# Performance work log

Hardware: AMD Instinct MI355X
Metric: run time of the kernel (lower is better)

Reference implementation:

```python
import jax, jax.numpy as jnp
import numpy as np
import math

_DENSE_LOCAL_W = 64
_DYADIC = [96, 128, 192, 256, 384, 512, 768, 1024, 1536]
OFFSETS = sorted(set(range(0, _DENSE_LOCAL_W + 1)) | set(_DYADIC))  # 74 offsets

B, N, D, H = 1, 2048, 1024, 16
HD = D // H


def setup_inputs() -> dict:
    key = jax.random.key(0)
    ks = jax.random.split(key, 8)
    s = 1.0 / math.sqrt(D)
    x = jax.random.normal(ks[0], (B, N, D), dtype=jnp.float32)
    Wqkv = jax.random.uniform(ks[1], (3 * D, D), jnp.float32, -s, s)
    bqkv = jax.random.uniform(ks[2], (3 * D,), jnp.float32, -s, s)
    Wgate = jax.random.uniform(ks[3], (D, D), jnp.float32, -s, s)
    bgate = jax.random.uniform(ks[4], (D,), jnp.float32, -s, s)
    Wout = jax.random.uniform(ks[5], (D, D), jnp.float32, -s, s)
    bout = jax.random.uniform(ks[6], (D,), jnp.float32, -s, s)
    # pos_bias init exactly as in the module: -log(1+delta) * alpha_h, shape (O, H)
    alphas = jnp.linspace(0.2, 2.0, H)
    deltas = jnp.array([math.log(1.0 + d) for d in OFFSETS], dtype=jnp.float32)
    pos_bias = -deltas[:, None] * alphas[None, :]
    offsets = jnp.array(OFFSETS, dtype=jnp.int32)
    return {"x": x, "Wqkv": Wqkv, "bqkv": bqkv, "Wgate": Wgate, "bgate": bgate,
            "Wout": Wout, "bout": bout, "pos_bias": pos_bias, "offsets": offsets}


def reference(x, Wqkv, bqkv, Wgate, bgate, Wout, bout, pos_bias, offsets):
    Bx, Nx, Dx = x.shape
    qkv = x @ Wqkv.T + bqkv                       # (B, N, 3D)
    q, k, v = jnp.split(qkv, 3, axis=-1)
    q = q.reshape(Bx, Nx, H, HD).transpose(0, 2, 1, 3)  # (B, H, N, HD)
    k = k.reshape(Bx, Nx, H, HD).transpose(0, 2, 1, 3)
    v = v.reshape(Bx, Nx, H, HD).transpose(0, 2, 1, 3)
    scale = HD ** -0.5

    # gather shifted K/V: position n attends to n - delta for each fixed offset
    n_idx = jnp.arange(Nx, dtype=jnp.int32)[:, None]      # (N, 1)
    idx = n_idx - offsets[None, :]                        # (N, O)
    valid = idx >= 0                                      # (N, O)
    idx_c = jnp.clip(idx, 0, Nx - 1)
    K_all = k[:, :, idx_c, :]                             # (B, H, N, O, HD)
    V_all = v[:, :, idx_c, :]

    scores = jnp.einsum('bhnd,bhnod->bhno', q, K_all) * scale
    scores = scores + pos_bias.T[None, :, None, :]        # (1, H, 1, O)
    scores = jnp.where(valid[None, None], scores, -jnp.inf)
    alpha = jax.nn.softmax(scores, axis=-1)               # (B, H, N, O)
    out = jnp.einsum('bhno,bhnod->bhnd', alpha, V_all)    # (B, H, N, HD)

    flat = out.transpose(0, 2, 1, 3).reshape(Bx, Nx, Dx)  # (B, N, D)
    gate = jax.nn.sigmoid(x @ Wgate.T + bgate)
    return (flat * gate) @ Wout.T + bout                  # dropout = identity (eval)
```

## Files before the change

### kernel.cpp

```cpp
#include <hip/hip_runtime.h>
#include <hip/hip_bf16.h>

#define SEQ_N 2048
#define DIM   1024
#define NHEAD 16
#define HDIM  64
#define LDQ   4096
#define NOFF  74
#define NDENSE 65
#define NJ    224
#define NT    16
#define PST   232
#define QST   88

typedef __attribute__((ext_vector_type(8))) __bf16 bv8;
typedef __attribute__((ext_vector_type(4))) __bf16 bv4;
typedef __attribute__((ext_vector_type(4))) float  f32x4;

typedef __attribute__((address_space(3))) void as3_void;
typedef __attribute__((address_space(1))) void as1_void;

__device__ __forceinline__ void async16(const void* g, void* l) {
  __builtin_amdgcn_global_load_lds((as1_void*)(unsigned long long)g,
                                   (as3_void*)l, 16, 0, 0);
}

#define E1 (SEQ_N * DIM)
#define E2 (E1 + 3 * DIM * DIM)
#define E3 (E2 + DIM * DIM)
#define E4 (E3 + DIM * DIM)
__global__ __launch_bounds__(256) void cvt_all(
    const float* __restrict__ x, const float* __restrict__ wqkv,
    const float* __restrict__ wgate, const float* __restrict__ wout,
    __bf16* __restrict__ dst) {
  long i = ((long)blockIdx.x * 256 + threadIdx.x) * 4;
  if (i >= E4) return;
  const float* s; long o;
  if (i < E1)      { s = x;     o = i; }
  else if (i < E2) { s = wqkv;  o = i - E1; }
  else if (i < E3) { s = wgate; o = i - E2; }
  else             { s = wout;  o = i - E3; }
  float4 v = *(const float4*)(s + o);
  bv4 ov;
  ov[0] = (__bf16)v.x; ov[1] = (__bf16)v.y; ov[2] = (__bf16)v.z; ov[3] = (__bf16)v.w;
  *(bv4*)(dst + i) = ov;
}

#define BM 128
#define BKT 128

template <int BN_, typename OutT>
__global__ __launch_bounds__(256) void gemm_bt(
    const __bf16* __restrict__ A, const __bf16* __restrict__ B1,
    const __bf16* __restrict__ B2, const float* __restrict__ bias1,
    const float* __restrict__ bias2, int Nsplit,
    OutT* __restrict__ C, int ldc, int K) {
  __shared__ __attribute__((aligned(16))) __bf16 Asm[BM * BKT];
  __shared__ __attribute__((aligned(16))) __bf16 Bsm[BN_ * BKT];
  constexpr int NJT = BN_ / 32;
  constexpr int CA = BM * BKT / 8;
  constexpr int CB = BN_ * BKT / 8;
  constexpr int CPR = BKT / 8;

  const int tid  = threadIdx.x;
  const int lane = tid & 63;
  const int wave = tid >> 6;
  const int wr = wave >> 1, wc = wave & 1;
  const int fr = lane & 15, fq = lane >> 4;
  const int fr7 = fr & 7;

  const int bn0 = blockIdx.x * BN_;
  const int bm0 = blockIdx.y * BM;

  const __bf16* Bp;
  const float* biasp;
  if (bn0 < Nsplit) { Bp = B1 + (size_t)bn0 * K;            biasp = bias1 + bn0; }
  else              { Bp = B2 + (size_t)(bn0 - Nsplit) * K; biasp = bias2 + (bn0 - Nsplit); }
  const __bf16* Ap = A + (size_t)bm0 * K;

  f32x4 acc[4][NJT] = {};

  for (int kt = 0; kt < K; kt += BKT) {
    __syncthreads();
#pragma unroll
    for (int c0 = 0; c0 < CA + CB; c0 += 256) {
      int c = c0 + tid;
      if (c < CA) {
        int rr = c / CPR, qq = c % CPR;
        int qs = qq ^ (rr & 7);
        async16(Ap + (size_t)rr * K + kt + qs * 8, Asm + c * 8);
      } else {
        int cb = c - CA;
        int rr = cb / CPR, qq = cb % CPR;
        int qs = qq ^ (rr & 7);
        async16(Bp + (size_t)rr * K + kt + qs * 8, Bsm + cb * 8);
      }
    }
    __syncthreads();

#pragma unroll
    for (int kk = 0; kk < BKT / 32; ++kk) {
      const int qs = ((kk * 4 + fq) ^ fr7) * 8;
      bv8 af[4], bfr[NJT];
#pragma unroll
      for (int i = 0; i < 4; ++i)
        af[i] = *(const bv8*)(Asm + (wr * 64 + i * 16 + fr) * BKT + qs);
#pragma unroll
      for (int j = 0; j < NJT; ++j)
        bfr[j] = *(const bv8*)(Bsm + (wc * (BN_ / 2) + j * 16 + fr) * BKT + qs);
#pragma unroll
      for (int i = 0; i < 4; ++i)
#pragma unroll
        for (int j = 0; j < NJT; ++j)
          acc[i][j] = __builtin_amdgcn_mfma_f32_16x16x32_bf16(af[i], bfr[j], acc[i][j], 0, 0, 0);
    }
  }

#pragma unroll
  for (int i = 0; i < 4; ++i) {
#pragma unroll
    for (int j = 0; j < NJT; ++j) {
      int ccol = wc * (BN_ / 2) + j * 16 + fr;
      float b = biasp[ccol];
#pragma unroll
      for (int r = 0; r < 4; ++r) {
        int row = bm0 + wr * 64 + i * 16 + fq * 4 + r;
        C[(size_t)row * ldc + bn0 + ccol] = (OutT)(acc[i][j][r] + b);
      }
    }
  }
}

#define BKG 64
template <typename OutT>
__global__ __launch_bounds__(256) void gemm_bt64(
    const __bf16* __restrict__ A, const __bf16* __restrict__ B,
    const float* __restrict__ bias, OutT* __restrict__ C, int ldc, int K) {
  __shared__ __attribute__((aligned(16))) __bf16 Asm[64 * BKG];
  __shared__ __attribute__((aligned(16))) __bf16 Bsm[64 * BKG];

  const int tid  = threadIdx.x;
  const int lane = tid & 63;
  const int wave = tid >> 6;
  const int wr = wave >> 1, wc = wave & 1;
  const int fr = lane & 15, fq = lane >> 4;
  const int fr7 = fr & 7;

  const int bn0 = blockIdx.x * 64;
  const int bm0 = blockIdx.y * 64;

  const __bf16* Ap = A + (size_t)bm0 * K;
  const __bf16* Bp = B + (size_t)bn0 * K;
  const float* biasp = bias + bn0;

  f32x4 acc[2][2] = {};

  for (int kt = 0; kt < K; kt += BKG) {
    __syncthreads();
#pragma unroll
    for (int c0 = 0; c0 < 512; c0 += 256) {
      int c = c0 + tid;
      int rr = c >> 3, qq = c & 7;
      int qs = qq ^ (rr & 7);
      async16(Ap + (size_t)rr * K + kt + qs * 8, Asm + c * 8);
      async16(Bp + (size_t)rr * K + kt + qs * 8, Bsm + c * 8);
    }
    __syncthreads();

#pragma unroll
    for (int kk = 0; kk < 2; ++kk) {
      const int qs = ((kk * 4 + fq) ^ fr7) * 8;
      bv8 af[2], bfr[2];
#pragma unroll
      for (int i = 0; i < 2; ++i)
        af[i] = *(const bv8*)(Asm + (wr * 32 + i * 16 + fr) * BKG + qs);
#pragma unroll
      for (int j = 0; j < 2; ++j)
        bfr[j] = *(const bv8*)(Bsm + (wc * 32 + j * 16 + fr) * BKG + qs);
#pragma unroll
      for (int i = 0; i < 2; ++i)
#pragma unroll
        for (int j = 0; j < 2; ++j)
          acc[i][j] = __builtin_amdgcn_mfma_f32_16x16x32_bf16(af[i], bfr[j], acc[i][j], 0, 0, 0);
    }
  }

#pragma unroll
  for (int i = 0; i < 2; ++i) {
#pragma unroll
    for (int j = 0; j < 2; ++j) {
      int ccol = wc * 32 + j * 16 + fr;
      float b = biasp[ccol];
#pragma unroll
      for (int r = 0; r < 4; ++r) {
        int row = bm0 + wr * 32 + i * 16 + fq * 4 + r;
        C[(size_t)row * ldc + bn0 + ccol] = (OutT)(acc[i][j][r] + b);
      }
    }
  }
}

__global__ __launch_bounds__(256) void attn_mfma(
    const __bf16* __restrict__ qkv,
    const float* __restrict__ pos_bias,
    const int* __restrict__ offsets,
    __bf16* __restrict__ fg) {
  const int n0 = (blockIdx.x >> 4) * NT;
  const int h  = blockIdx.x & 15;
  const int tid = threadIdx.x;
  const int lane = tid & 63;
  const int w = tid >> 6;
  const int fr = lane & 15, fq = lane >> 4;
  const int fr7 = fr & 7;

  __shared__ __attribute__((aligned(16))) __bf16 Kbuf[NJ * HDIM];
  __shared__ __attribute__((aligned(16))) __bf16 Vbuf[NJ * HDIM];
  __shared__ __attribute__((aligned(16))) __bf16 Qbuf[NT * QST];
  __shared__ __attribute__((aligned(16))) float  Sbuf[NT][80];
  __shared__ __attribute__((aligned(16))) __bf16 Pd[NT * PST];
  __shared__ float inv_l[NT];

  if (tid < 128) {
    int ni = tid >> 3, ch = tid & 7;
    bv8 q = *(const bv8*)(qkv + (size_t)(n0 + ni) * LDQ + h * HDIM + ch * 8);
    *(bv8*)(Qbuf + ni * QST + ch * 8) = q;
  }
#pragma unroll
  for (int c0 = 0; c0 < NT * PST / 8; c0 += 256) {
    int c = c0 + tid;
    if (c < NT * PST / 8) *(uint4*)(Pd + c * 8) = make_uint4(0, 0, 0, 0);
  }
  {
    int ch = lane & 7;
    int rowin = lane >> 3;
    int chs = ch ^ rowin;
#pragma unroll
    for (int it = 0; it < 7; ++it) {
      int jbase = it * 32 + w * 8;
      int j = jbase + rowin;
      int g;
      if (j < 80) g = n0 - 64 + j;
      else { int jj = j - 80; g = n0 - offsets[NDENSE + (jj >> 4)] + (jj & 15); }
      if (g < 0) g = 0;
      const __bf16* base = qkv + (size_t)g * LDQ + DIM + h * HDIM;
      async16(base + chs * 8, Kbuf + jbase * HDIM + lane * 8);
      async16(base + DIM + ch * 8, Vbuf + jbase * HDIM + lane * 8);
    }
  }
  __syncthreads();

  for (int jb = w; jb < 14; jb += 4) {
    f32x4 acc = {};
#pragma unroll
    for (int kk = 0; kk < 2; ++kk) {
      bv8 a = *(const bv8*)(Qbuf + fr * QST + kk * 32 + fq * 8);
      bv8 b = *(const bv8*)(Kbuf + (jb * 16 + fr) * HDIM + ((kk * 4 + fq) ^ fr7) * 8);
      acc = __builtin_amdgcn_mfma_f32_16x16x32_bf16(a, b, acc, 0, 0, 0);
    }
    int j = jb * 16 + fr;
    if (jb < 5) {
      bool gvalid = (n0 - 64 + j) >= 0;
#pragma unroll
      for (int r = 0; r < 4; ++r) {
        int ni = fq * 4 + r;
        int o = ni + 64 - j;
        if (o >= 0 && o < NDENSE)
          Sbuf[ni][o] = gvalid ? acc[r] : -3.0e38f;
      }
    } else {
      int jj = j - 80;
      int s = jj >> 4, tni = jj & 15;
      int r = tni - fq * 4;
      if (r >= 0 && r < 4) {
        bool gvalid = (n0 + tni - offsets[NDENSE + s]) >= 0;
        Sbuf[tni][NDENSE + s] = gvalid ? acc[r] : -3.0e38f;
      }
    }
  }
  __syncthreads();

  {
    int t = tid & 15, ni = tid >> 4;
    float sc5[5];
    float m = -3.0e38f;
#pragma unroll
    for (int k = 0; k < 5; ++k) {
      int o = t + k * 16;
      float v = -3.0e38f;
      if (o < NOFF) {
        float raw = Sbuf[ni][o];
        if (raw > -1.0e38f) v = raw * 0.125f + pos_bias[o * NHEAD + h];
      }
      sc5[k] = v;
      m = fmaxf(m, v);
    }
#pragma unroll
    for (int d = 1; d < 16; d <<= 1) m = fmaxf(m, __shfl_xor(m, d));
    float sum = 0.f;
#pragma unroll
    for (int k = 0; k < 5; ++k) {
      int o = t + k * 16;
      if (o < NOFF && sc5[k] > -1.0e38f) {
        float e = __expf(sc5[k] - m);
        sum += e;
        int j = (o < NDENSE) ? (ni + 64 - o) : (80 + (o - NDENSE) * 16 + ni);
        Pd[ni * PST + j] = (__bf16)e;
      }
    }
#pragma unroll
    for (int d = 1; d < 16; d <<= 1) sum += __shfl_xor(sum, d);
    if (t == 0) inv_l[ni] = 1.f / sum;
  }
  __syncthreads();

  {
    const int db = w;
    f32x4 acc = {};
#pragma unroll
    for (int kt = 0; kt < 7; ++kt) {
      bv8 a = *(const bv8*)(Pd + fr * PST + kt * 32 + fq * 8);
      bv8 b;
#pragma unroll
      for (int jj = 0; jj < 8; ++jj)
        b[jj] = Vbuf[(kt * 32 + fq * 8 + jj) * HDIM + db * 16 + fr];
      acc = __builtin_amdgcn_mfma_f32_16x16x32_bf16(a, b, acc, 0, 0, 0);
    }
    int d = db * 16 + fr;
#pragma unroll
    for (int r = 0; r < 4; ++r) {
      int ni = fq * 4 + r;
      float o = acc[r] * inv_l[ni];
      float gp = (float)qkv[(size_t)(n0 + ni) * LDQ + 3 * DIM + h * HDIM + d];
      float gate = 1.f / (1.f + __expf(-gp));
      fg[(size_t)(n0 + ni) * DIM + h * HDIM + d] = (__bf16)(o * gate);
    }
  }
}

extern "C" void kernel_launch(void* const* d_in, const int* in_sizes, int n_in,
                              void* d_out, int out_size, void* d_ws, size_t ws_size,
                              hipStream_t stream) {
  const float* x        = (const float*)d_in[0];
  const float* Wqkv     = (const float*)d_in[1];
  const float* bqkv     = (const float*)d_in[2];
  const float* Wgate    = (const float*)d_in[3];
  const float* bgate    = (const float*)d_in[4];
  const float* Wout     = (const float*)d_in[5];
  const float* bout     = (const float*)d_in[6];
  const float* pos_bias = (const float*)d_in[7];
  const int*   offsets  = (const int*)d_in[8];
  float* out = (float*)d_out;

  __bf16* xb       = (__bf16*)d_ws;
  __bf16* Wqkvb    = xb    + (size_t)SEQ_N * DIM;
  __bf16* Wgateb   = Wqkvb + (size_t)3 * DIM * DIM;
  __bf16* Woutb    = Wgateb + (size_t)DIM * DIM;
  __bf16* qkvg     = Woutb + (size_t)DIM * DIM;
  __bf16* flatgate = qkvg + (size_t)SEQ_N * LDQ;

  cvt_all<<<dim3(E4 / 1024), dim3(256), 0, stream>>>(x, Wqkv, Wgate, Wout, xb);

  gemm_bt<128, __bf16><<<dim3(LDQ / 128, SEQ_N / BM), dim3(256), 0, stream>>>(
      xb, Wqkvb, Wgateb, bqkv, bgate, 3 * DIM, qkvg, LDQ, DIM);

  attn_mfma<<<dim3((SEQ_N / NT) * NHEAD), dim3(256), 0, stream>>>(
      qkvg, pos_bias, offsets, flatgate);

  gemm_bt64<float><<<dim3(DIM / 64, SEQ_N / 64), dim3(256), 0, stream>>>(
      flatgate, Woutb, bout, out, DIM, DIM);
}
```

Before: 144.4 us.

## Reuse one LDS buffer for K then V in attention to raise occupancy

The attention kernel now keeps K and V in a single shared-memory buffer. K is loaded first for the QK^T MFMAs, and after the score barrier V is asynchronously loaded into the same buffer while softmax runs. This roughly halves the kernel's LDS footprint so more blocks can be resident per CU, but V-load latency is now only partly hidden behind softmax. The small-tile GEMM's K-step is also switched from a local constant to the shared BKT tile depth.

```diff
diff --git a/kernel.cpp b/kernel.cpp
--- a/kernel.cpp
+++ b/kernel.cpp
@@ -131,13 +131,14 @@
   }
 }
 
-#define BKG 64
 template <typename OutT>
 __global__ __launch_bounds__(256) void gemm_bt64(
     const __bf16* __restrict__ A, const __bf16* __restrict__ B,
     const float* __restrict__ bias, OutT* __restrict__ C, int ldc, int K) {
-  __shared__ __attribute__((aligned(16))) __bf16 Asm[64 * BKG];
-  __shared__ __attribute__((aligned(16))) __bf16 Bsm[64 * BKG];
+  __shared__ __attribute__((aligned(16))) __bf16 Asm[64 * BKT];
+  __shared__ __attribute__((aligned(16))) __bf16 Bsm[64 * BKT];
+  constexpr int CM = 64 * BKT / 8;
+  constexpr int CPR = BKT / 8;
 
   const int tid  = threadIdx.x;
   const int lane = tid & 63;
@@ -155,12 +156,12 @@
 
   f32x4 acc[2][2] = {};
 
-  for (int kt = 0; kt < K; kt += BKG) {
+  for (int kt = 0; kt < K; kt += BKT) {
     __syncthreads();
 #pragma unroll
-    for (int c0 = 0; c0 < 512; c0 += 256) {
+    for (int c0 = 0; c0 < CM; c0 += 256) {
       int c = c0 + tid;
-      int rr = c >> 3, qq = c & 7;
+      int rr = c / CPR, qq = c % CPR;
       int qs = qq ^ (rr & 7);
       async16(Ap + (size_t)rr * K + kt + qs * 8, Asm + c * 8);
       async16(Bp + (size_t)rr * K + kt + qs * 8, Bsm + c * 8);
@@ -168,15 +169,15 @@
     __syncthreads();
 
 #pragma unroll
-    for (int kk = 0; kk < 2; ++kk) {
+    for (int kk = 0; kk < BKT / 32; ++kk) {
       const int qs = ((kk * 4 + fq) ^ fr7) * 8;
       bv8 af[2], bfr[2];
 #pragma unroll
       for (int i = 0; i < 2; ++i)
-        af[i] = *(const bv8*)(Asm + (wr * 32 + i * 16 + fr) * BKG + qs);
+        af[i] = *(const bv8*)(Asm + (wr * 32 + i * 16 + fr) * BKT + qs);
 #pragma unroll
       for (int j = 0; j < 2; ++j)
-        bfr[j] = *(const bv8*)(Bsm + (wc * 32 + j * 16 + fr) * BKG + qs);
+        bfr[j] = *(const bv8*)(Bsm + (wc * 32 + j * 16 + fr) * BKT + qs);
 #pragma unroll
       for (int i = 0; i < 2; ++i)
 #pragma unroll
@@ -213,17 +214,19 @@
   const int fr = lane & 15, fq = lane >> 4;
   const int fr7 = fr & 7;
 
-  __shared__ __attribute__((aligned(16))) __bf16 Kbuf[NJ * HDIM];
-  __shared__ __attribute__((aligned(16))) __bf16 Vbuf[NJ * HDIM];
+  __shared__ __attribute__((aligned(16))) __bf16 KVbuf[NJ * HDIM];
   __shared__ __attribute__((aligned(16))) __bf16 Qbuf[NT * QST];
   __shared__ __attribute__((aligned(16))) float  Sbuf[NT][80];
   __shared__ __attribute__((aligned(16))) __bf16 Pd[NT * PST];
   __shared__ float inv_l[NT];
 
+  const int ch = lane & 7;
+  const int rowin = lane >> 3;
+
   if (tid < 128) {
-    int ni = tid >> 3, ch = tid & 7;
-    bv8 q = *(const bv8*)(qkv + (size_t)(n0 + ni) * LDQ + h * HDIM + ch * 8);
-    *(bv8*)(Qbuf + ni * QST + ch * 8) = q;
+    int ni = tid >> 3, cq = tid & 7;
+    bv8 q = *(const bv8*)(qkv + (size_t)(n0 + ni) * LDQ + h * HDIM + cq * 8);
+    *(bv8*)(Qbuf + ni * QST + cq * 8) = q;
   }
 #pragma unroll
   for (int c0 = 0; c0 < NT * PST / 8; c0 += 256) {
@@ -231,8 +234,6 @@
     if (c < NT * PST / 8) *(uint4*)(Pd + c * 8) = make_uint4(0, 0, 0, 0);
   }
   {
-    int ch = lane & 7;
-    int rowin = lane >> 3;
     int chs = ch ^ rowin;
 #pragma unroll
     for (int it = 0; it < 7; ++it) {
@@ -242,9 +243,8 @@
       if (j < 80) g = n0 - 64 + j;
       else { int jj = j - 80; g = n0 - offsets[NDENSE + (jj >> 4)] + (jj & 15); }
       if (g < 0) g = 0;
-      const __bf16* base = qkv + (size_t)g * LDQ + DIM + h * HDIM;
-      async16(base + chs * 8, Kbuf + jbase * HDIM + lane * 8);
-      async16(base + DIM + ch * 8, Vbuf + jbase * HDIM + lane * 8);
+      async16(qkv + (size_t)g * LDQ + DIM + h * HDIM + chs * 8,
+              KVbuf + jbase * HDIM + lane * 8);
     }
   }
   __syncthreads();
@@ -254,7 +254,7 @@
 #pragma unroll
     for (int kk = 0; kk < 2; ++kk) {
       bv8 a = *(const bv8*)(Qbuf + fr * QST + kk * 32 + fq * 8);
-      bv8 b = *(const bv8*)(Kbuf + (jb * 16 + fr) * HDIM + ((kk * 4 + fq) ^ fr7) * 8);
+      bv8 b = *(const bv8*)(KVbuf + (jb * 16 + fr) * HDIM + ((kk * 4 + fq) ^ fr7) * 8);
       acc = __builtin_amdgcn_mfma_f32_16x16x32_bf16(a, b, acc, 0, 0, 0);
     }
     int j = jb * 16 + fr;
@@ -279,6 +279,18 @@
   }
   __syncthreads();
 
+#pragma unroll
+  for (int it = 0; it < 7; ++it) {
+    int jbase = it * 32 + w * 8;
+    int j = jbase + rowin;
+    int g;
+    if (j < 80) g = n0 - 64 + j;
+    else { int jj = j - 80; g = n0 - offsets[NDENSE + (jj >> 4)] + (jj & 15); }
+    if (g < 0) g = 0;
+    async16(qkv + (size_t)g * LDQ + 2 * DIM + h * HDIM + ch * 8,
+            KVbuf + jbase * HDIM + lane * 8);
+  }
+
   {
     int t = tid & 15, ni = tid >> 4;
     float sc5[5];
@@ -322,7 +334,7 @@
       bv8 b;
 #pragma unroll
       for (int jj = 0; jj < 8; ++jj)
-        b[jj] = Vbuf[(kt * 32 + fq * 8 + jj) * HDIM + db * 16 + fr];
+        b[jj] = KVbuf[(kt * 32 + fq * 8 + jj) * HDIM + db * 16 + fr];
       acc = __builtin_amdgcn_mfma_f32_16x16x32_bf16(a, b, acc, 0, 0, 0);
     }
     int d = db * 16 + fr;
```

Measured after the change: 141.1 us. 1.02x faster.
